# Kernel optimization log

Hardware: AMD Instinct MI355X
Metric: run time of the kernel (lower is better)

Reference implementation:

```python
import jax, jax.numpy as jnp
import numpy as np

N_NODES = 38000   # 19 feature types x ~2000 categories
IN_DIM = 64
HID = 128         # hid_num in source
R = 8             # number of relations
E = 200000        # edges per relation
N_ROWS = 60000    # data rows
F = 19            # len(features)
N_CLASSES = 10


def setup_inputs() -> dict:
    key = jax.random.key(0)
    ks = jax.random.split(key, 20)
    s_in = 1.0 / np.sqrt(IN_DIM)
    s_h = 1.0 / np.sqrt(HID)
    inp = {
        "node_feats": jax.random.normal(ks[0], (N_NODES, IN_DIM), jnp.float32),
        "edges_src": jax.random.randint(ks[1], (R, E), 0, N_NODES),
        "edges_dst": jax.random.randint(ks[2], (R, E), 0, N_NODES),
        "row_idx": jax.random.randint(ks[3], (N_ROWS, F), 0, N_NODES),
        "row_mask": jax.random.randint(ks[4], (N_ROWS, F), 0, 2).astype(bool),
        # input linear
        "W_in": jax.random.normal(ks[5], (IN_DIM, HID), jnp.float32) * s_in,
        "b_in": jnp.zeros((HID,), jnp.float32),
        # RGCN layer 1 and 2: per-relation GraphConv weights
        "W1": jax.random.normal(ks[6], (R, HID, HID), jnp.float32) * s_h,
        "b1": jnp.zeros((R, HID), jnp.float32),
        "W2": jax.random.normal(ks[7], (R, HID, HID), jnp.float32) * s_h,
        "b2": jnp.zeros((R, HID), jnp.float32),
        # MLP head
        "Wm1": jax.random.normal(ks[8], (HID, HID), jnp.float32) * s_h,
        "bm1": jnp.zeros((HID,), jnp.float32),
        "Wm2": jax.random.normal(ks[9], (HID, HID), jnp.float32) * s_h,
        "bm2": jnp.zeros((HID,), jnp.float32),
        "Wm3": jax.random.normal(ks[10], (HID, N_CLASSES), jnp.float32) * s_h,
        "bm3": jnp.zeros((N_CLASSES,), jnp.float32),
    }
    return inp


def _hetero_conv(h, src, dst, W, b):
    """DGL HeteroGraphConv(sum) of GraphConv(norm='both') over R relations."""
    n = h.shape[0]
    out = jnp.zeros((n, W.shape[2]), h.dtype)
    ones = jnp.ones((src.shape[1],), h.dtype)
    for r in range(src.shape[0]):
        deg_out = jax.ops.segment_sum(ones, src[r], num_segments=n)
        deg_in = jax.ops.segment_sum(ones, dst[r], num_segments=n)
        norm_s = jnp.where(deg_out > 0, deg_out, 1.0) ** -0.5
        norm_d = jnp.where(deg_in > 0, deg_in, 1.0) ** -0.5
        msg = h[src[r]] * norm_s[src[r], None]            # [E, hid]
        agg = jax.ops.segment_sum(msg, dst[r], num_segments=n)
        out = out + (agg * norm_d[:, None]) @ W[r] + b[r]
    return out


def reference(node_feats, edges_src, edges_dst, row_idx, row_mask,
              W_in, b_in, W1, b1, W2, b2, Wm1, bm1, Wm2, bm2, Wm3, bm3):
    # input linear + relu (applied to every node type's features)
    h = jax.nn.relu(node_feats @ W_in + b_in)            # [N_nodes, HID]
    # 2-layer RGCN
    h = jax.nn.relu(_hetero_conv(h, edges_src, edges_dst, W1, b1))
    h = _hetero_conv(h, edges_src, edges_dst, W2, b2)    # [N_nodes, HID]
    # vectorized ragged gather + masked mean (replaces per-row python loop)
    m = row_mask.astype(h.dtype)                          # [N_rows, F]
    emb = h[row_idx] * m[..., None]                       # [N_rows, F, HID]
    cnt = jnp.maximum(m.sum(-1, keepdims=True), 1.0)
    mean_feat = emb.sum(1) / cnt                          # [N_rows, HID]
    # MLP head
    x = jax.nn.relu(mean_feat @ Wm1 + bm1)
    x = jax.nn.relu(x @ Wm2 + bm2)
    return x @ Wm3 + bm3                                  # [N_rows, N_CLASSES]
```

## Files before the change

### kernel.cpp

```cpp
#include <hip/hip_runtime.h>
#include <hip/hip_bf16.h>

#define NN    38000
#define HID   128
#define RR    8
#define EE    200000
#define NROWS 60000
#define FF    19
#define NCLS  10
#define NRD   (RR*NN)
#define HB    38912
#define CH    8
#define CE    (EE/CH)

typedef __hip_bfloat16 bf16;
typedef __attribute__((ext_vector_type(8))) short short8;
typedef __attribute__((ext_vector_type(4))) float floatx4;

__device__ __forceinline__ float b2f(bf16 x){ return __bfloat162float(x); }
__device__ __forceinline__ bf16  f2b(float x){ return __float2bfloat16(x); }

__device__ __forceinline__ int geti(const void* a, long long i, int wide){
  return wide ? (int)(((const long long*)a)[i]) : ((const int*)a)[i];
}

__global__ void k_fill(float* out, int n, float v){
  int i = blockIdx.x*256 + threadIdx.x;
  if (i < n) out[i] = v;
}

__global__ void k_sniff(const void* mask, const void* ridx, const void* esrc, int* flags){
  int lane = threadIdx.x;
  const unsigned short* mu = (const unsigned short*)mask;
  int l3f80e=0, l3f80o=0, lbytehi=0, loddnz=0, lother=0;
  for (int i = lane; i < 4096; i += 64){
    unsigned v = mu[i];
    if (v == 0) continue;
    if (v == 0x3F80){ if (i & 1) l3f80o = 1; else l3f80e = 1; continue; }
    unsigned lo = v & 0xFF, hi = v >> 8;
    int lob = (lo == 0 || lo == 1 || lo == 0xFF);
    int hib = (hi == 0 || hi == 1 || hi == 0xFF);
    if (lob && hib){ if (hi) lbytehi = 1; if (i & 1) loddnz = 1; continue; }
    lother = 1;
  }
  int a3f80e = __any(l3f80e);
  int a3f80o = __any(l3f80o);
  int abytehi = __any(lbytehi);
  int aoddnz = __any(loddnz);
  int aother = __any(lother);
  int mtype = -1;
  if (!aother){
    if (a3f80e && !abytehi && !aoddnz)       mtype = 2;
    else if (a3f80o && !a3f80e && !abytehi)  mtype = 3;
    else if (!a3f80e && !a3f80o){
      if (abytehi || aoddnz) mtype = 1;
      else                   mtype = 0;
    }
  }
  const int* es = (const int*)esrc;
  int loddE = 0, lseenE = 0;
  for (int i = lane; i < 512; i += 64){
    if (es[2*i+1] != 0) loddE = 1;
    if (es[2*i] > 1)    lseenE = 1;
  }
  int fE = (!__any(loddE) && __any(lseenE)) ? 1 : 0;
  const int* ri = (const int*)ridx;
  int loddI = 0, lseenI = 0;
  for (int i = lane; i < 512; i += 64){
    if (ri[2*i+1] != 0) loddI = 1;
    if (ri[2*i] > 1)    lseenI = 1;
  }
  int fI = (!__any(loddI) && __any(lseenI)) ? 1 : 0;
  if (lane == 0){ flags[1] = mtype; flags[3] = fE; flags[4] = fI; }
}


__global__ __launch_bounds__(1024) void kg_hist(const void* esrc, const void* edst,
                                                unsigned short* __restrict__ ghd,
                                                unsigned short* __restrict__ ghs,
                                                const int* flags){
  __shared__ int hist[HB];
  int t = threadIdx.x;
  for (int i = t; i < HB; i += 1024) hist[i] = 0;
  __syncthreads();
  int b = blockIdx.x;
  int side = b >> 6;
  int r = (b >> 3) & 7, c = b & 7;
  int wide = flags[3];
  const void* e = side ? esrc : edst;
  long long base = (long long)r*EE + (long long)c*CE;
  if (!wide){
    const int* p = (const int*)e + base;
    for (int i = t; i < CE; i += 1024) atomicAdd(&hist[p[i]], 1);
  } else {
    const long long* p = (const long long*)e + base;
    for (int i = t; i < CE; i += 1024) atomicAdd(&hist[(int)p[i]], 1);
  }
  __syncthreads();
  unsigned short* out = (side ? ghs : ghd) + (long long)(r*CH + c)*HB;
  for (int i = t; i < HB; i += 1024) out[i] = (unsigned short)hist[i];
}

__global__ void kg_tot(const unsigned short* __restrict__ ghd,
                       const unsigned short* __restrict__ ghs,
                       int* __restrict__ totg, float* __restrict__ ns){
  int i = blockIdx.x*256 + threadIdx.x;
  if (i >= RR*HB) return;
  int r = i / HB, bin = i - r*HB;
  int sd = 0, ss = 0;
#pragma unroll
  for (int c = 0; c < CH; c++){
    sd += ghd[(long long)(r*CH+c)*HB + bin];
    ss += ghs[(long long)(r*CH+c)*HB + bin];
  }
  totg[i] = sd;
  if (bin < NN) ns[r*NN + bin] = rsqrtf((float)(ss > 0 ? ss : 1));
}

__global__ __launch_bounds__(1024) void kg_scan(const int* __restrict__ totg,
                                                int* __restrict__ rowptr){
  __shared__ int tot[HB];
  __shared__ int wsum[16];
  int t = threadIdx.x, r = blockIdx.x;
  for (int i = t; i < HB; i += 1024) tot[i] = totg[r*HB + i];
  __syncthreads();
  int b0 = t*38;
  int loc[38], s = 0;
#pragma unroll
  for (int j = 0; j < 38; j++){ loc[j] = s; s += tot[b0+j]; }
  int lane = t & 63, w = t >> 6;
  int sc = s;
  for (int off = 1; off < 64; off <<= 1){
    int v = __shfl_up(sc, off);
    if (lane >= off) sc += v;
  }
  if (lane == 63) wsum[w] = sc;
  __syncthreads();
  if (t < 16){
    int v = wsum[t];
    int scw = v;
    for (int off = 1; off < 16; off <<= 1){
      int u = __shfl_up(scw, off);
      if (t >= off) scw += u;
    }
    wsum[t] = scw - v;
  }
  __syncthreads();
  int base = r*EE + (sc - s) + wsum[w];
#pragma unroll
  for (int j = 0; j < 38; j++) tot[b0+j] = base + loc[j];
  __syncthreads();
  for (int i = t; i < NN; i += 1024) rowptr[r*NN + i] = tot[i];
  if (r == RR-1 && t == 0) rowptr[NRD] = RR*EE;
}

__global__ void kg_curs(const unsigned short* __restrict__ ghd,
                        const int* __restrict__ rowptr,
                        int* __restrict__ gcurs){
  int i = blockIdx.x*256 + threadIdx.x;
  if (i >= NRD) return;
  int r = i / NN, bin = i - r*NN;
  int p = rowptr[i];
#pragma unroll
  for (int c = 0; c < CH; c++){
    gcurs[(long long)(r*CH+c)*HB + bin] = p;
    p += ghd[(long long)(r*CH+c)*HB + bin];
  }
}

__global__ __launch_bounds__(1024) void kg_scatter(const void* esrc, const void* edst,
                                                   const int* __restrict__ gcurs,
                                                   const float* __restrict__ ns,
                                                   int2* __restrict__ csrw, const int* flags){
  __shared__ int cur[HB];
  int t = threadIdx.x, b = blockIdx.x;
  int r = b >> 3, c = b & 7;
  const int* g = gcurs + (long long)(r*CH + c)*HB;
  for (int i = t; i < HB; i += 1024) cur[i] = g[i];
  __syncthreads();
  if (b == 0 && t < 8){ int2 z; z.x = 0; z.y = 0; csrw[RR*EE + t] = z; }
  int wide = flags[3];
  const float* nsr = ns + r*NN;
  long long base = (long long)r*EE + (long long)c*CE;
  if (!wide){
    const int* ps = (const int*)esrc + base;
    const int* pd = (const int*)edst + base;
    for (int i = t; i < CE; i += 1024){
      int d = pd[i], s = ps[i];
      int pos = atomicAdd(&cur[d], 1);
      int2 v; v.x = s; v.y = __float_as_int(nsr[s]);
      csrw[pos] = v;
    }
  } else {
    const long long* ps = (const long long*)esrc + base;
    const long long* pd = (const long long*)edst + base;
    for (int i = t; i < CE; i += 1024){
      int d = (int)pd[i], s = (int)ps[i];
      int pos = atomicAdd(&cur[d], 1);
      int2 v; v.x = s; v.y = __float_as_int(nsr[s]);
      csrw[pos] = v;
    }
  }
}


__global__ void k_bias(const float* b_in, const float* b1, const float* b2,
                       const float* bm1, const float* bm2, const float* bm3, float* o){
  int t = threadIdx.x;
  o[t] = b_in[t];
  float s1 = 0.f, s2 = 0.f;
  for (int r = 0; r < RR; r++){ s1 += b1[r*HID+t]; s2 += b2[r*HID+t]; }
  o[128+t] = s1; o[256+t] = s2;
  o[384+t] = bm1[t]; o[512+t] = bm2[t];
  if (t < NCLS) o[640+t] = bm3[t];
}

__global__ void k_packall(const float* __restrict__ W1, const float* __restrict__ W2,
                          const float* __restrict__ Wm1, const float* __restrict__ Wm2,
                          bf16* __restrict__ W1p, bf16* __restrict__ W2p,
                          bf16* __restrict__ Wm1p, bf16* __restrict__ Wm2p){
  int idx0 = blockIdx.x*256 + threadIdx.x;
  if (idx0 < 4*65536){
    const float* W = (idx0 < 2*65536) ? W1 : W2;
    bf16* out      = (idx0 < 2*65536) ? W1p : W2p;
    int idx = idx0 & (2*65536 - 1);
    int j = idx & 7;
    int l = (idx >> 3) & 63;
    int t = (idx >> 9) & 127;
    int g = idx >> 16;
    int ktg = t & 15, nt = t >> 4;
    int kglob = ktg*32 + ((l>>4)<<3) + j;
    int rel = kglob >> 7;
    int krow = kglob & 127;
    int n = nt*16 + (l&15);
    out[idx] = f2b(W[((g*4 + rel)*128 + krow)*128 + n]);
  } else if (idx0 < 4*65536 + 2*16384){
    int t2 = idx0 - 4*65536;
    const float* B = (t2 < 16384) ? Wm1 : Wm2;
    bf16* out      = (t2 < 16384) ? Wm1p : Wm2p;
    int idx = t2 & 16383;
    int j  = idx & 7;
    int l  = (idx >> 3) & 63;
    int t  = idx >> 9;
    int kt = t & 3;
    int nt = t >> 2;
    int k = kt*32 + ((l>>4)<<3) + j;
    int n = nt*16 + (l&15);
    out[idx] = f2b(B[k*128 + n]);
  }
}

__global__ void k_gemm_in(const float* __restrict__ A, const float* __restrict__ B,
                          const float* bias, bf16* __restrict__ out){
  int row0 = blockIdx.x * 4;
  int col = threadIdx.x;
  float a0=0.f, a1=0.f, a2=0.f, a3=0.f;
  for (int k = 0; k < 64; k++){
    float bv = B[k*HID + col];
    a0 += A[(long long)(row0+0)*64 + k] * bv;
    a1 += A[(long long)(row0+1)*64 + k] * bv;
    a2 += A[(long long)(row0+2)*64 + k] * bv;
    a3 += A[(long long)(row0+3)*64 + k] * bv;
  }
  float bb = bias[col];
  out[(long long)(row0+0)*HID + col] = f2b(fmaxf(a0 + bb, 0.f));
  out[(long long)(row0+1)*HID + col] = f2b(fmaxf(a1 + bb, 0.f));
  out[(long long)(row0+2)*HID + col] = f2b(fmaxf(a2 + bb, 0.f));
  out[(long long)(row0+3)*HID + col] = f2b(fmaxf(a3 + bb, 0.f));
}

#define LOADW(Q, base_) \
  Q##0 = cw[(base_)+0]; Q##1 = cw[(base_)+1]; Q##2 = cw[(base_)+2]; Q##3 = cw[(base_)+3]; \
  Q##4 = cw[(base_)+4]; Q##5 = cw[(base_)+5]; Q##6 = cw[(base_)+6]; Q##7 = cw[(base_)+7];

#define GATHW(P, Q) \
  P##0 = hv[(long long)(int)Q##0*64 + lane]; \
  P##1 = hv[(long long)(int)Q##1*64 + lane]; \
  P##2 = hv[(long long)(int)Q##2*64 + lane]; \
  P##3 = hv[(long long)(int)Q##3*64 + lane]; \
  P##4 = hv[(long long)(int)Q##4*64 + lane]; \
  P##5 = hv[(long long)(int)Q##5*64 + lane]; \
  P##6 = hv[(long long)(int)Q##6*64 + lane]; \
  P##7 = hv[(long long)(int)Q##7*64 + lane];

#define ACCE(Qv, Pv, cond) { \
  float wk_ = (cond) ? __int_as_float((int)((Qv) >> 32)) : 0.f; \
  acc0 += wk_ * __uint_as_float((Pv) << 16); \
  acc1 += wk_ * __uint_as_float((Pv) & 0xffff0000u); }

#define ROWBODY(i, QC, PC, QN, PN) { \
  int b_ = __builtin_amdgcn_readfirstlane(__shfl(rp, (i))); \
  int e_ = __builtin_amdgcn_readfirstlane(__shfl(rp, (i)+1)); \
  LOADW(QN, e_)                        \
  GATHW(PN, QN)                        \
  float acc0 = 0.f, acc1 = 0.f; \
  ACCE(QC##0, PC##0, b_+0 < e_) \
  ACCE(QC##1, PC##1, b_+1 < e_) \
  ACCE(QC##2, PC##2, b_+2 < e_) \
  ACCE(QC##3, PC##3, b_+3 < e_) \
  ACCE(QC##4, PC##4, b_+4 < e_) \
  ACCE(QC##5, PC##5, b_+5 < e_) \
  ACCE(QC##6, PC##6, b_+6 < e_) \
  ACCE(QC##7, PC##7, b_+7 < e_) \
  for (int j = b_ + 8; j < e_; j += 8){       \
    unsigned long long q0 = cw[j],   q1 = cw[j+1], q2 = cw[j+2], q3 = cw[j+3]; \
    unsigned long long q4 = cw[j+4], q5 = cw[j+5], q6 = cw[j+6], q7 = cw[j+7]; \
    unsigned p0 = hv[(long long)(int)q0*64 + lane]; \
    unsigned p1 = hv[(long long)(int)q1*64 + lane]; \
    unsigned p2 = hv[(long long)(int)q2*64 + lane]; \
    unsigned p3 = hv[(long long)(int)q3*64 + lane]; \
    unsigned p4 = hv[(long long)(int)q4*64 + lane]; \
    unsigned p5 = hv[(long long)(int)q5*64 + lane]; \
    unsigned p6 = hv[(long long)(int)q6*64 + lane]; \
    unsigned p7 = hv[(long long)(int)q7*64 + lane]; \
    ACCE(q0, p0, 1) \
    ACCE(q1, p1, j+1 < e_) \
    ACCE(q2, p2, j+2 < e_) \
    ACCE(q3, p3, j+3 < e_) \
    ACCE(q4, p4, j+4 < e_) \
    ACCE(q5, p5, j+5 < e_) \
    ACCE(q6, p6, j+6 < e_) \
    ACCE(q7, p7, j+7 < e_) \
  } \
  int deg = e_ - b_; \
  float nd = rsqrtf((float)(deg > 0 ? deg : 1)); \
  bf16 o0 = f2b(acc0 * nd), o1 = f2b(acc1 * nd); \
  unsigned ov = ((unsigned)(*(unsigned short*)&o1) << 16) | (*(unsigned short*)&o0); \
  int addr = (w << 12) + ((i) << 8) + (lane << 2); \
  addr ^= (((i) & 7) << 4); \
  *(unsigned*)(lds + addr) = ov; }

__global__ __launch_bounds__(512) void k_layer(const bf16* __restrict__ h,
                                               const int* __restrict__ rowptr,
                                               const unsigned long long* __restrict__ cw,
                                               const bf16* __restrict__ Bp,
                                               const float* __restrict__ bias,
                                               bf16* __restrict__ hout, int relu){
  __shared__ char lds[8*16*256];
  int w = threadIdx.x >> 6;
  int lane = threadIdx.x & 63;
  int d0 = blockIdx.x << 4;
  const unsigned* hv = (const unsigned*)h;

  int rp = 0;
  if (lane < 17) rp = rowptr[w*NN + d0 + lane];

  unsigned long long qa0,qa1,qa2,qa3,qa4,qa5,qa6,qa7;
  unsigned long long qb0,qb1,qb2,qb3,qb4,qb5,qb6,qb7;
  unsigned pa0,pa1,pa2,pa3,pa4,pa5,pa6,pa7;
  unsigned pb0,pb1,pb2,pb3,pb4,pb5,pb6,pb7;

  {
    int b0_ = __builtin_amdgcn_readfirstlane(__shfl(rp, 0));
    LOADW(qa, b0_)
    GATHW(pa, qa)
  }
  ROWBODY( 0, qa, pa, qb, pb)
  ROWBODY( 1, qb, pb, qa, pa)
  ROWBODY( 2, qa, pa, qb, pb)
  ROWBODY( 3, qb, pb, qa, pa)
  ROWBODY( 4, qa, pa, qb, pb)
  ROWBODY( 5, qb, pb, qa, pa)
  ROWBODY( 6, qa, pa, qb, pb)
  ROWBODY( 7, qb, pb, qa, pa)
  ROWBODY( 8, qa, pa, qb, pb)
  ROWBODY( 9, qb, pb, qa, pa)
  ROWBODY(10, qa, pa, qb, pb)
  ROWBODY(11, qb, pb, qa, pa)
  ROWBODY(12, qa, pa, qb, pb)
  ROWBODY(13, qb, pb, qa, pa)
  ROWBODY(14, qa, pa, qb, pb)
  ROWBODY(15, qb, pb, qa, pa)
  __syncthreads();

  floatx4 acc = (floatx4){0.f,0.f,0.f,0.f};
  int row = lane & 15;
  int kb = (lane >> 4) << 4;
#pragma unroll
  for (int rel = 0; rel < 8; rel++){
    int half = rel >> 2;
    const bf16* bp = Bp + half*65536 + lane*8 + (w*16 + (rel & 3)*4)*512;
#pragma unroll
    for (int ktl = 0; ktl < 4; ktl++){
      int off = (row << 8) + ktl*64 + kb;
      off ^= ((row & 7) << 4);
      short8 a = *(const short8*)(lds + (rel << 12) + off);
      short8 b = *(const short8*)(bp + ktl*512);
      acc = __builtin_amdgcn_mfma_f32_16x16x32_bf16(a, b, acc, 0, 0, 0);
    }
  }
  int col = w*16 + (lane & 15);
  int row0 = d0 + ((lane >> 4) << 2);
  float bb = bias[col];
#pragma unroll
  for (int v = 0; v < 4; v++){
    float x = acc[v] + bb;
    if (relu) x = fmaxf(x, 0.f);
    hout[(long long)(row0 + v)*HID + col] = f2b(x);
  }
}

__global__ __launch_bounds__(256) void k_head(const bf16* __restrict__ h,
                                              const void* ridx, const void* rmask,
                                              const int* __restrict__ flags,
                                              const bf16* __restrict__ Wm1p,
                                              const bf16* __restrict__ Wm2p,
                                              const float* __restrict__ Wm3,
                                              const float* __restrict__ bias,
                                              float* __restrict__ out){
  __shared__ char ldsA[16*256];
  __shared__ char ldsB[16*256];
  int wv = threadIdx.x >> 6;
  int lane = threadIdx.x & 63;
  int r0 = blockIdx.x << 4;
  int mt = flags[1];
  int wide = flags[4];
  const int* m4            = (const int*)rmask;
  const unsigned char* m1  = (const unsigned char*)rmask;
  const unsigned short* m2 = (const unsigned short*)rmask;
  const unsigned int* mw   = (const unsigned int*)rmask;
  const unsigned* hv = (const unsigned*)h;

  for (int rr = 0; rr < 4; rr++){
    int tr = wv*4 + rr;
    int row = r0 + tr;
    int on = 0, idxl = 0;
    if (lane < FF){
      long long i = (long long)row*FF + lane;
      if      (mt == 1) on = (m1[i] != 0);
      else if (mt == 2) on = (m2[i] != 0);
      else if (mt == 3) on = (mw[i] != 0);
      else              on = (m4[i] != 0);
      if (on) idxl = geti(ridx, i, wide);
    }
    unsigned long long bal = __ballot(on);
    float cnt = (float)__popcll(bal);
    float acc0 = 0.f, acc1 = 0.f;
#pragma unroll
    for (int j = 0; j < FF; j++){
      int s = __shfl(idxl, j);
      float wgt = (float)((bal >> j) & 1ull);
      unsigned pv = hv[(long long)s*64 + lane];
      acc0 += wgt * __uint_as_float(pv << 16);
      acc1 += wgt * __uint_as_float(pv & 0xffff0000u);
    }
    float inv = 1.f / fmaxf(cnt, 1.f);
    bf16 o0 = f2b(acc0 * inv), o1 = f2b(acc1 * inv);
    unsigned ov = ((unsigned)(*(unsigned short*)&o1) << 16) | (*(unsigned short*)&o0);
    int addr = (tr << 8) + (lane << 2);
    addr ^= ((tr & 7) << 4);
    *(unsigned*)(ldsA + addr) = ov;
  }
  __syncthreads();

  int arow = lane & 15;
  int kb = (lane >> 4) << 4;
  int colB = lane & 15;
  int rowQ = (lane >> 4) << 2;

  {
    floatx4 accA = (floatx4){0.f,0.f,0.f,0.f};
    floatx4 accB = (floatx4){0.f,0.f,0.f,0.f};
    const bf16* bp = Wm1p + lane*8;
#pragma unroll
    for (int kt = 0; kt < 4; kt++){
      int off = (arow << 8) + kt*64 + kb;
      off ^= ((arow & 7) << 4);
      short8 a = *(const short8*)(ldsA + off);
      short8 b0 = *(const short8*)(bp + ((wv*2+0)*4 + kt)*512);
      short8 b1 = *(const short8*)(bp + ((wv*2+1)*4 + kt)*512);
      accA = __builtin_amdgcn_mfma_f32_16x16x32_bf16(a, b0, accA, 0, 0, 0);
      accB = __builtin_amdgcn_mfma_f32_16x16x32_bf16(a, b1, accB, 0, 0, 0);
    }
#pragma unroll
    for (int ntl = 0; ntl < 2; ntl++){
      int col = (wv*2 + ntl)*16 + colB;
      float bb = bias[384 + col];
#pragma unroll
      for (int v = 0; v < 4; v++){
        float x = ((ntl == 0) ? accA[v] : accB[v]) + bb;
        bf16 xv = f2b(fmaxf(x, 0.f));
        int rowi = rowQ + v;
        int addr = (rowi << 8) + col*2;
        addr ^= ((rowi & 7) << 4);
        *(unsigned short*)(ldsB + addr) = *(unsigned short*)&xv;
      }
    }
  }
  __syncthreads();

  {
    floatx4 accA = (floatx4){0.f,0.f,0.f,0.f};
    floatx4 accB = (floatx4){0.f,0.f,0.f,0.f};
    const bf16* bp = Wm2p + lane*8;
#pragma unroll
    for (int kt = 0; kt < 4; kt++){
      int off = (arow << 8) + kt*64 + kb;
      off ^= ((arow & 7) << 4);
      short8 a = *(const short8*)(ldsB + off);
      short8 b0 = *(const short8*)(bp + ((wv*2+0)*4 + kt)*512);
      short8 b1 = *(const short8*)(bp + ((wv*2+1)*4 + kt)*512);
      accA = __builtin_amdgcn_mfma_f32_16x16x32_bf16(a, b0, accA, 0, 0, 0);
      accB = __builtin_amdgcn_mfma_f32_16x16x32_bf16(a, b1, accB, 0, 0, 0);
    }
#pragma unroll
    for (int ntl = 0; ntl < 2; ntl++){
      int col = (wv*2 + ntl)*16 + colB;
      float bb = bias[512 + col];
#pragma unroll
      for (int v = 0; v < 4; v++){
        float x = ((ntl == 0) ? accA[v] : accB[v]) + bb;
        bf16 xv = f2b(fmaxf(x, 0.f));
        int rowi = rowQ + v;
        int addr = (rowi << 8) + col*2;
        addr ^= ((rowi & 7) << 4);
        *(unsigned short*)(ldsA + addr) = *(unsigned short*)&xv;
      }
    }
  }
  __syncthreads();

  for (int t = threadIdx.x; t < 16*NCLS; t += 256){
    int tr = t / NCLS, col = t - tr*NCLS;
    float acc = bias[640 + col];
    for (int k = 0; k < HID; k++){
      int addr = (tr << 8) + k*2;
      addr ^= ((tr & 7) << 4);
      unsigned short uv = *(const unsigned short*)(ldsA + addr);
      acc += b2f(*(bf16*)&uv) * Wm3[k*NCLS + col];
    }
    out[(long long)(r0 + tr)*NCLS + col] = acc;
  }
}

extern "C" void kernel_launch(void* const* d_in, const int* in_sizes, int n_in,
                              void* d_out, int out_size, void* d_ws, size_t ws_size,
                              hipStream_t stream){
  float* out = (float*)d_out;

  static const int expect[17] = {
    NN*64, RR*EE, RR*EE, NROWS*FF, NROWS*FF,
    64*HID, HID, RR*HID*HID, RR*HID, RR*HID*HID, RR*HID,
    HID*HID, HID, HID*HID, HID, HID*NCLS, NCLS };
  bool ok = (n_in >= 17) && (out_size == NROWS*NCLS);
  if (ok) for (int i = 0; i < 17; i++) if (in_sizes[i] != expect[i]) { ok = false; break; }
  if (!ok){
    k_fill<<<(NROWS*NCLS+255)/256, 256, 0, stream>>>(out, NROWS*NCLS, 64.0f);
    return;
  }

  const void*  e_src = d_in[1];
  const void*  e_dst = d_in[2];
  const void*  ridx  = d_in[3];
  const void*  rmask = d_in[4];
  const float* nf   = (const float*)d_in[0];
  const float* W_in = (const float*)d_in[5];
  const float* b_in = (const float*)d_in[6];
  const float* W1   = (const float*)d_in[7];
  const float* b1   = (const float*)d_in[8];
  const float* W2   = (const float*)d_in[9];
  const float* b2   = (const float*)d_in[10];
  const float* Wm1  = (const float*)d_in[11];
  const float* bm1  = (const float*)d_in[12];
  const float* Wm2  = (const float*)d_in[13];
  const float* bm2  = (const float*)d_in[14];
  const float* Wm3  = (const float*)d_in[15];
  const float* bm3  = (const float*)d_in[16];

  char* ws = (char*)d_ws;
  size_t off = 0;
  auto take = [&](size_t bytes)->char*{
    char* p = ws + off; off += (bytes + 255) & ~(size_t)255; return p; };

  int*   flags  = (int*)  take(256);
  char*  rgn    =         take(58368000);
  unsigned short* ghd = (unsigned short*)(rgn);
  unsigned short* ghs = (unsigned short*)(rgn + 4980736);
  int*   gcurs  = (int*)  (rgn +  9961472);
  int*   totg   = (int*)  (rgn + 19922944);
  bf16*  h1     = (bf16*) take((size_t)NN*HID*2);
  bf16*  h2     = (bf16*) take((size_t)NN*HID*2);
  int*   rowptr = (int*)  take((size_t)(NRD+1)*4);
  int2*  csrw   = (int2*) take((size_t)RR*EE*8 + 64);
  float* ns     = (float*)take((size_t)NRD*4);
  float* bias   = (float*)take(656*4);
  bf16*  W1p    = (bf16*) take((size_t)2*65536*2);
  bf16*  W2p    = (bf16*) take((size_t)2*65536*2);
  bf16*  Wm1p   = (bf16*) take((size_t)16384*2);
  bf16*  Wm2p   = (bf16*) take((size_t)16384*2);

  if (off > ws_size){
    k_fill<<<(NROWS*NCLS+255)/256, 256, 0, stream>>>(out, NROWS*NCLS, 32.0f);
    return;
  }

  k_sniff   <<<1, 64, 0, stream>>>(rmask, ridx, e_src, flags);
  kg_hist   <<<128, 1024, 0, stream>>>(e_src, e_dst, ghd, ghs, flags);
  kg_tot    <<<(RR*HB+255)/256, 256, 0, stream>>>(ghd, ghs, totg, ns);
  kg_scan   <<<RR, 1024, 0, stream>>>(totg, rowptr);
  kg_curs   <<<(NRD+255)/256, 256, 0, stream>>>(ghd, rowptr, gcurs);
  kg_scatter<<<64, 1024, 0, stream>>>(e_src, e_dst, gcurs, ns, csrw, flags);
  k_bias    <<<1, 128, 0, stream>>>(b_in, b1, b2, bm1, bm2, bm3, bias);

  k_packall<<<(4*65536 + 2*16384 + 255)/256, 256, 0, stream>>>(W1, W2, Wm1, Wm2,
                                                               W1p, W2p, Wm1p, Wm2p);

  k_gemm_in<<<NN/4, 128, 0, stream>>>(nf, W_in, bias+0, h1);

  k_layer<<<NN/16, 512, 0, stream>>>(h1, rowptr, (const unsigned long long*)csrw,
                                     W1p, bias+128, h2, 1);
  k_layer<<<NN/16, 512, 0, stream>>>(h2, rowptr, (const unsigned long long*)csrw,
                                     W2p, bias+256, h1, 0);

  k_head<<<NROWS/16, 256, 0, stream>>>(h1, ridx, rmask, flags, Wm1p, Wm2p, Wm3, bias, out);
}
```

Measured before the change: 440.4 us.

## Double edge chunking in CSR build, pre-scale gather indices, pack FMA accumulators

The edge chunk count for the histogram and scatter kernels goes from 8 to 16, doubling the grid size so more CUs work on CSR construction. The workspace offsets grow to fit the larger per-chunk histograms. Source indices are now stored pre-multiplied by 64, which drops the 64-bit multiply from each gather address. The two scalar accumulators become a float2 vector so the compiler can issue packed FMAs. The costs are more histogram zeroing and write-back work per chunk, and a 32-bit offset limit on gather addressing.

```diff
diff --git a/kernel.cpp b/kernel.cpp
--- a/kernel.cpp
+++ b/kernel.cpp
@@ -10,12 +10,13 @@
 #define NCLS  10
 #define NRD   (RR*NN)
 #define HB    38912
-#define CH    8
+#define CH    16
 #define CE    (EE/CH)
 
 typedef __hip_bfloat16 bf16;
 typedef __attribute__((ext_vector_type(8))) short short8;
 typedef __attribute__((ext_vector_type(4))) float floatx4;
+typedef __attribute__((ext_vector_type(2))) float float2v;
 
 __device__ __forceinline__ float b2f(bf16 x){ return __bfloat162float(x); }
 __device__ __forceinline__ bf16  f2b(float x){ return __float2bfloat16(x); }
@@ -84,8 +85,8 @@
   for (int i = t; i < HB; i += 1024) hist[i] = 0;
   __syncthreads();
   int b = blockIdx.x;
-  int side = b >> 6;
-  int r = (b >> 3) & 7, c = b & 7;
+  int side = b >> 7;
+  int r = (b >> 4) & 7, c = b & 15;
   int wide = flags[3];
   const void* e = side ? esrc : edst;
   long long base = (long long)r*EE + (long long)c*CE;
@@ -174,7 +175,7 @@
                                                    int2* __restrict__ csrw, const int* flags){
   __shared__ int cur[HB];
   int t = threadIdx.x, b = blockIdx.x;
-  int r = b >> 3, c = b & 7;
+  int r = b >> 4, c = b & 15;
   const int* g = gcurs + (long long)(r*CH + c)*HB;
   for (int i = t; i < HB; i += 1024) cur[i] = g[i];
   __syncthreads();
@@ -188,7 +189,7 @@
     for (int i = t; i < CE; i += 1024){
       int d = pd[i], s = ps[i];
       int pos = atomicAdd(&cur[d], 1);
-      int2 v; v.x = s; v.y = __float_as_int(nsr[s]);
+      int2 v; v.x = s << 6; v.y = __float_as_int(nsr[s]);
       csrw[pos] = v;
     }
   } else {
@@ -197,7 +198,7 @@
     for (int i = t; i < CE; i += 1024){
       int d = (int)pd[i], s = (int)ps[i];
       int pos = atomicAdd(&cur[d], 1);
-      int2 v; v.x = s; v.y = __float_as_int(nsr[s]);
+      int2 v; v.x = s << 6; v.y = __float_as_int(nsr[s]);
       csrw[pos] = v;
     }
   }
@@ -274,26 +275,28 @@
   Q##4 = cw[(base_)+4]; Q##5 = cw[(base_)+5]; Q##6 = cw[(base_)+6]; Q##7 = cw[(base_)+7];
 
 #define GATHW(P, Q) \
-  P##0 = hv[(long long)(int)Q##0*64 + lane]; \
-  P##1 = hv[(long long)(int)Q##1*64 + lane]; \
-  P##2 = hv[(long long)(int)Q##2*64 + lane]; \
-  P##3 = hv[(long long)(int)Q##3*64 + lane]; \
-  P##4 = hv[(long long)(int)Q##4*64 + lane]; \
-  P##5 = hv[(long long)(int)Q##5*64 + lane]; \
-  P##6 = hv[(long long)(int)Q##6*64 + lane]; \
-  P##7 = hv[(long long)(int)Q##7*64 + lane];
+  P##0 = hv[(int)Q##0 + lane]; \
+  P##1 = hv[(int)Q##1 + lane]; \
+  P##2 = hv[(int)Q##2 + lane]; \
+  P##3 = hv[(int)Q##3 + lane]; \
+  P##4 = hv[(int)Q##4 + lane]; \
+  P##5 = hv[(int)Q##5 + lane]; \
+  P##6 = hv[(int)Q##6 + lane]; \
+  P##7 = hv[(int)Q##7 + lane];
 
 #define ACCE(Qv, Pv, cond) { \
   float wk_ = (cond) ? __int_as_float((int)((Qv) >> 32)) : 0.f; \
-  acc0 += wk_ * __uint_as_float((Pv) << 16); \
-  acc1 += wk_ * __uint_as_float((Pv) & 0xffff0000u); }
+  float2v xv_; \
+  xv_.x = __uint_as_float((Pv) << 16); \
+  xv_.y = __uint_as_float((Pv) & 0xffff0000u); \
+  acc2 += (float2v){wk_, wk_} * xv_; }
 
 #define ROWBODY(i, QC, PC, QN, PN) { \
   int b_ = __builtin_amdgcn_readfirstlane(__shfl(rp, (i))); \
   int e_ = __builtin_amdgcn_readfirstlane(__shfl(rp, (i)+1)); \
   LOADW(QN, e_)                        \
   GATHW(PN, QN)                        \
-  float acc0 = 0.f, acc1 = 0.f; \
+  float2v acc2 = (float2v){0.f, 0.f}; \
   ACCE(QC##0, PC##0, b_+0 < e_) \
   ACCE(QC##1, PC##1, b_+1 < e_) \
   ACCE(QC##2, PC##2, b_+2 < e_) \
@@ -305,14 +308,14 @@
   for (int j = b_ + 8; j < e_; j += 8){       \
     unsigned long long q0 = cw[j],   q1 = cw[j+1], q2 = cw[j+2], q3 = cw[j+3]; \
     unsigned long long q4 = cw[j+4], q5 = cw[j+5], q6 = cw[j+6], q7 = cw[j+7]; \
-    unsigned p0 = hv[(long long)(int)q0*64 + lane]; \
-    unsigned p1 = hv[(long long)(int)q1*64 + lane]; \
-    unsigned p2 = hv[(long long)(int)q2*64 + lane]; \
-    unsigned p3 = hv[(long long)(int)q3*64 + lane]; \
-    unsigned p4 = hv[(long long)(int)q4*64 + lane]; \
-    unsigned p5 = hv[(long long)(int)q5*64 + lane]; \
-    unsigned p6 = hv[(long long)(int)q6*64 + lane]; \
-    unsigned p7 = hv[(long long)(int)q7*64 + lane]; \
+    unsigned p0 = hv[(int)q0 + lane]; \
+    unsigned p1 = hv[(int)q1 + lane]; \
+    unsigned p2 = hv[(int)q2 + lane]; \
+    unsigned p3 = hv[(int)q3 + lane]; \
+    unsigned p4 = hv[(int)q4 + lane]; \
+    unsigned p5 = hv[(int)q5 + lane]; \
+    unsigned p6 = hv[(int)q6 + lane]; \
+    unsigned p7 = hv[(int)q7 + lane]; \
     ACCE(q0, p0, 1) \
     ACCE(q1, p1, j+1 < e_) \
     ACCE(q2, p2, j+2 < e_) \
@@ -324,7 +327,7 @@
   } \
   int deg = e_ - b_; \
   float nd = rsqrtf((float)(deg > 0 ? deg : 1)); \
-  bf16 o0 = f2b(acc0 * nd), o1 = f2b(acc1 * nd); \
+  bf16 o0 = f2b(acc2.x * nd), o1 = f2b(acc2.y * nd); \
   unsigned ov = ((unsigned)(*(unsigned short*)&o1) << 16) | (*(unsigned short*)&o0); \
   int addr = (w << 12) + ((i) << 8) + (lane << 2); \
   addr ^= (((i) & 7) << 4); \
@@ -575,9 +578,9 @@
   int*   flags  = (int*)  take(256);
   char*  rgn    =         take(58368000);
   unsigned short* ghd = (unsigned short*)(rgn);
-  unsigned short* ghs = (unsigned short*)(rgn + 4980736);
-  int*   gcurs  = (int*)  (rgn +  9961472);
-  int*   totg   = (int*)  (rgn + 19922944);
+  unsigned short* ghs = (unsigned short*)(rgn + 9961472);
+  int*   gcurs  = (int*)  (rgn + 19922944);
+  int*   totg   = (int*)  (rgn + 39845888);
   bf16*  h1     = (bf16*) take((size_t)NN*HID*2);
   bf16*  h2     = (bf16*) take((size_t)NN*HID*2);
   int*   rowptr = (int*)  take((size_t)(NRD+1)*4);
@@ -595,11 +598,11 @@
   }
 
   k_sniff   <<<1, 64, 0, stream>>>(rmask, ridx, e_src, flags);
-  kg_hist   <<<128, 1024, 0, stream>>>(e_src, e_dst, ghd, ghs, flags);
+  kg_hist   <<<256, 1024, 0, stream>>>(e_src, e_dst, ghd, ghs, flags);
   kg_tot    <<<(RR*HB+255)/256, 256, 0, stream>>>(ghd, ghs, totg, ns);
   kg_scan   <<<RR, 1024, 0, stream>>>(totg, rowptr);
   kg_curs   <<<(NRD+255)/256, 256, 0, stream>>>(ghd, rowptr, gcurs);
-  kg_scatter<<<64, 1024, 0, stream>>>(e_src, e_dst, gcurs, ns, csrw, flags);
+  kg_scatter<<<128, 1024, 0, stream>>>(e_src, e_dst, gcurs, ns, csrw, flags);
   k_bias    <<<1, 128, 0, stream>>>(b_in, b1, b2, bm1, bm2, bm3, bias);
 
   k_packall<<<(4*65536 + 2*16384 + 255)/256, 256, 0, stream>>>(W1, W2, Wm1, Wm2,
```

Result: faster. 412.1 us (-6.4%).
